# Kernel optimization log

Hardware: AMD Instinct MI355X
Metric: run time of the kernel (lower is better)

The kernel has to match this reference:

```python
import jax, jax.numpy as jnp
import numpy as np

B, S, D = 256, 512, 256
ATT = 128

def setup_inputs() -> dict:
    key = jax.random.key(0)
    k1, k2, k3, k4 = jax.random.split(key, 4)
    x = jax.random.normal(k1, (B, S, D), dtype=jnp.float32)
    W = jax.random.normal(k2, (D, ATT), dtype=jnp.float32)
    b = jax.random.normal(k3, (ATT,), dtype=jnp.float32)
    u = jax.random.normal(k4, (ATT, 1), dtype=jnp.float32)
    return {"x": x, "W": W, "b": b, "u": u}

def reference(x, W, b, u):
    # uit: [B, S, ATT]
    uit = jnp.tanh(jnp.einsum('bsd,da->bsa', x, W) + b)
    # scores: [B, S]  (faithful: exp without max-subtraction, as in original)
    ait = jnp.exp(jnp.einsum('bsa,a->bs', uit, u[:, 0]))
    ait = ait / (jnp.sum(ait, axis=1, keepdims=True) + 1e-08)
    # weighted sum over seq -> [B, D]
    return jnp.einsum('bsd,bs->bd', x, ait)
```

## Files before the change

### kernel.cpp

```cpp
#include <hip/hip_runtime.h>
#include <math.h>

typedef _Float16 f16x8 __attribute__((ext_vector_type(8)));
typedef float    f32x4 __attribute__((ext_vector_type(4)));

constexpr int B_ = 256, S_ = 512, D_ = 256, A_ = 128;
constexpr int BS = B_ * S_;

__device__ __forceinline__ float tanh_fast(float v) {
    return 1.0f - 2.0f / (1.0f + __expf(2.0f * v));
}

__global__ __launch_bounds__(512, 4) void k_scores(
    const float* __restrict__ x, const float* __restrict__ W,
    const float* __restrict__ bvec, const float* __restrict__ u,
    float* __restrict__ scores)
{
    __shared__ _Float16 xh[16 * 64 * 8];
    __shared__ _Float16 xl[16 * 64 * 8];
    __shared__ float    part[2][8][32];

    const int t    = threadIdx.x;
    const int lane = t & 63, wv = t >> 6;
    const int lr   = lane & 15, lg = lane >> 4;
    const int brow0 = blockIdx.x * 256;

    f16x8 Bh[8], Bl[8];
#pragma unroll
    for (int ks = 0; ks < 8; ++ks) {
        const float* wp = W + (size_t)(ks * 32 + lg * 8) * A_ + wv * 16 + lr;
#pragma unroll
        for (int i = 0; i < 8; ++i) {
            float v = wp[(size_t)i * A_];
            _Float16 h = (_Float16)v;
            Bh[ks][i] = h;
            Bl[ks][i] = (_Float16)(v - (float)h);
        }
    }
    const float bb = bvec[wv * 16 + lr];
    const float uu = u[wv * 16 + lr];

    float4 ld[2][2];

#define K1_ISSUE(TT)                                                              \
    {                                                                             \
        _Pragma("unroll")                                                         \
        for (int ff = 0; ff < 2; ++ff) {                                          \
            int f = wv * 2 + ff;                                                  \
            const float* p = x + (size_t)(brow0 + (TT) * 32 + ((f >> 3) << 4) + lr) * D_ \
                               + ((f & 7) << 5) + (lg << 3);                      \
            ld[ff][0] = *(const float4*)p;                                        \
            ld[ff][1] = *(const float4*)(p + 4);                                  \
        }                                                                         \
    }

#define K1_STAGE()                                                                \
    {                                                                             \
        _Pragma("unroll")                                                         \
        for (int ff = 0; ff < 2; ++ff) {                                          \
            int f = wv * 2 + ff;                                                  \
            float v[8] = {ld[ff][0].x, ld[ff][0].y, ld[ff][0].z, ld[ff][0].w,     \
                          ld[ff][1].x, ld[ff][1].y, ld[ff][1].z, ld[ff][1].w};    \
            f16x8 hi, lo;                                                         \
            _Pragma("unroll")                                                     \
            for (int i = 0; i < 8; ++i) {                                         \
                _Float16 h = (_Float16)v[i];                                      \
                hi[i] = h; lo[i] = (_Float16)(v[i] - (float)h);                   \
            }                                                                     \
            *(f16x8*)&xh[((size_t)f * 64 + lane) * 8] = hi;                       \
            *(f16x8*)&xl[((size_t)f * 64 + lane) * 8] = lo;                       \
        }                                                                         \
    }

    K1_ISSUE(0)
    K1_STAGE()

    for (int tt = 0; tt < 8; ++tt) {
        __syncthreads();
        if (tt > 0 && t < 32) {
            const float* pp = &part[(tt - 1) & 1][0][t];
            float ss = pp[0] + pp[32] + pp[64] + pp[96] + pp[128] + pp[160] + pp[192] + pp[224];
            scores[brow0 + (tt - 1) * 32 + t] = __expf(ss);
        }
        if (tt < 7) K1_ISSUE(tt + 1)

        f32x4 acc0 = {0.f, 0.f, 0.f, 0.f}, acc1 = {0.f, 0.f, 0.f, 0.f};
#pragma unroll
        for (int ks = 0; ks < 8; ++ks) {
            f16x8 ah0 = *(const f16x8*)&xh[((size_t)(ks) * 64 + lane) * 8];
            f16x8 al0 = *(const f16x8*)&xl[((size_t)(ks) * 64 + lane) * 8];
            f16x8 ah1 = *(const f16x8*)&xh[((size_t)(8 + ks) * 64 + lane) * 8];
            f16x8 al1 = *(const f16x8*)&xl[((size_t)(8 + ks) * 64 + lane) * 8];
            acc0 = __builtin_amdgcn_mfma_f32_16x16x32_f16(ah0, Bh[ks], acc0, 0, 0, 0);
            acc0 = __builtin_amdgcn_mfma_f32_16x16x32_f16(ah0, Bl[ks], acc0, 0, 0, 0);
            acc0 = __builtin_amdgcn_mfma_f32_16x16x32_f16(al0, Bh[ks], acc0, 0, 0, 0);
            acc1 = __builtin_amdgcn_mfma_f32_16x16x32_f16(ah1, Bh[ks], acc1, 0, 0, 0);
            acc1 = __builtin_amdgcn_mfma_f32_16x16x32_f16(ah1, Bl[ks], acc1, 0, 0, 0);
            acc1 = __builtin_amdgcn_mfma_f32_16x16x32_f16(al1, Bh[ks], acc1, 0, 0, 0);
        }
#pragma unroll
        for (int mt = 0; mt < 2; ++mt) {
            f32x4 a = mt ? acc1 : acc0;
#pragma unroll
            for (int r = 0; r < 4; ++r) {
                float s = tanh_fast(a[r] + bb) * uu;
                s += __shfl_xor(s, 8, 64);
                s += __shfl_xor(s, 4, 64);
                s += __shfl_xor(s, 2, 64);
                s += __shfl_xor(s, 1, 64);
                if (lr == 0) part[tt & 1][wv][mt * 16 + lg * 4 + r] = s;
            }
        }
        __syncthreads();
        if (tt < 7) K1_STAGE()
    }
    __syncthreads();
    if (t < 32) {
        const float* pp = &part[1][0][t];
        float ss = pp[0] + pp[32] + pp[64] + pp[96] + pp[128] + pp[160] + pp[192] + pp[224];
        scores[brow0 + 7 * 32 + t] = __expf(ss);
    }
#undef K1_ISSUE
#undef K1_STAGE
}

__global__ __launch_bounds__(512) void k_out(
    const float* __restrict__ x, const float* __restrict__ scores,
    float* __restrict__ out)
{
    __shared__ float sc[S_];
    __shared__ float red[8];
    __shared__ float pbuf[8][D_];

    const int t = threadIdx.x, b = blockIdx.x;
    const int lane = t & 63, w = t >> 6;

    float v = scores[(size_t)b * S_ + t];
    sc[t] = v;
    float rv = v;
#pragma unroll
    for (int m = 32; m >= 1; m >>= 1) rv += __shfl_xor(rv, m, 64);
    if (lane == 0) red[w] = rv;
    __syncthreads();

    const float* xp = x + ((size_t)b * S_ + (size_t)w * 64) * D_ + lane * 4;
    f32x4 a0 = {0.f, 0.f, 0.f, 0.f}, a1 = {0.f, 0.f, 0.f, 0.f};
#pragma unroll 8
    for (int j = 0; j < 64; j += 2) {
        float4 xa = *(const float4*)(xp + (size_t)j * D_);
        float4 xb = *(const float4*)(xp + (size_t)(j + 1) * D_);
        float s0 = sc[w * 64 + j], s1 = sc[w * 64 + j + 1];
        a0[0] = fmaf(xa.x, s0, a0[0]); a0[1] = fmaf(xa.y, s0, a0[1]);
        a0[2] = fmaf(xa.z, s0, a0[2]); a0[3] = fmaf(xa.w, s0, a0[3]);
        a1[0] = fmaf(xb.x, s1, a1[0]); a1[1] = fmaf(xb.y, s1, a1[1]);
        a1[2] = fmaf(xb.z, s1, a1[2]); a1[3] = fmaf(xb.w, s1, a1[3]);
    }
    a0[0] += a1[0]; a0[1] += a1[1]; a0[2] += a1[2]; a0[3] += a1[3];
    *(f32x4*)&pbuf[w][lane * 4] = a0;
    __syncthreads();

    if (t < D_) {
        float denom = 0.f;
#pragma unroll
        for (int i = 0; i < 8; ++i) denom += red[i];
        const float inv = 1.0f / (denom + 1e-8f);
        float r = 0.f;
#pragma unroll
        for (int i = 0; i < 8; ++i) r += pbuf[i][t];
        out[b * D_ + t] = r * inv;
    }
}

extern "C" void kernel_launch(void* const* d_in, const int* in_sizes, int n_in,
                              void* d_out, int out_size, void* d_ws, size_t ws_size,
                              hipStream_t stream)
{
    const float* x    = (const float*)d_in[0];
    const float* W    = (const float*)d_in[1];
    const float* bvec = (const float*)d_in[2];
    const float* u    = (const float*)d_in[3];
    float* out = (float*)d_out;
    float* scores = (float*)d_ws;

    k_scores<<<512, 512, 0, stream>>>(x, W, bvec, u, scores);
    k_out   <<<B_, 512, 0, stream>>>(x, scores, out);
}
```

Baseline: 224.5 us.

## Fuse score and weighted-sum kernels into one per-batch block

Merges the two kernels into one where each block handles a full batch row of 512 positions: it computes scores into shared memory, then normalises and does the weighted sum over x. This removes the global scores round trip and a kernel launch, and the second pass over x may hit in L2/MALL since the same block just read it. In exchange the grid shrinks from 512 to 256 blocks (one per batch) and the occupancy hint drops to 2, which lowers parallelism on a large GPU and may leave compute units idle.

```diff
diff --git a/kernel.cpp b/kernel.cpp
--- a/kernel.cpp
+++ b/kernel.cpp
@@ -5,25 +5,28 @@
 typedef float    f32x4 __attribute__((ext_vector_type(4)));
 
 constexpr int B_ = 256, S_ = 512, D_ = 256, A_ = 128;
-constexpr int BS = B_ * S_;
 
 __device__ __forceinline__ float tanh_fast(float v) {
     return 1.0f - 2.0f / (1.0f + __expf(2.0f * v));
 }
 
-__global__ __launch_bounds__(512, 4) void k_scores(
+__global__ __launch_bounds__(512, 2) void k_fused(
     const float* __restrict__ x, const float* __restrict__ W,
     const float* __restrict__ bvec, const float* __restrict__ u,
-    float* __restrict__ scores)
+    float* __restrict__ out)
 {
     __shared__ _Float16 xh[16 * 64 * 8];
     __shared__ _Float16 xl[16 * 64 * 8];
     __shared__ float    part[2][8][32];
+    __shared__ float    sc[S_];
+    __shared__ float    red[8];
+    __shared__ float    pbuf[8][D_];
 
     const int t    = threadIdx.x;
     const int lane = t & 63, wv = t >> 6;
     const int lr   = lane & 15, lg = lane >> 4;
-    const int brow0 = blockIdx.x * 256;
+    const int b    = blockIdx.x;
+    const float* __restrict__ xb = x + (size_t)b * S_ * D_;
 
     f16x8 Bh[8], Bl[8];
 #pragma unroll
@@ -47,8 +50,8 @@
         _Pragma("unroll")                                                         \
         for (int ff = 0; ff < 2; ++ff) {                                          \
             int f = wv * 2 + ff;                                                  \
-            const float* p = x + (size_t)(brow0 + (TT) * 32 + ((f >> 3) << 4) + lr) * D_ \
-                               + ((f & 7) << 5) + (lg << 3);                      \
+            const float* p = xb + (size_t)((TT) * 32 + ((f >> 3) << 4) + lr) * D_ \
+                                + ((f & 7) << 5) + (lg << 3);                     \
             ld[ff][0] = *(const float4*)p;                                        \
             ld[ff][1] = *(const float4*)(p + 4);                                  \
         }                                                                         \
@@ -75,14 +78,14 @@
     K1_ISSUE(0)
     K1_STAGE()
 
-    for (int tt = 0; tt < 8; ++tt) {
+    for (int tt = 0; tt < 16; ++tt) {
         __syncthreads();
         if (tt > 0 && t < 32) {
             const float* pp = &part[(tt - 1) & 1][0][t];
             float ss = pp[0] + pp[32] + pp[64] + pp[96] + pp[128] + pp[160] + pp[192] + pp[224];
-            scores[brow0 + (tt - 1) * 32 + t] = __expf(ss);
+            sc[(tt - 1) * 32 + t] = __expf(ss);
         }
-        if (tt < 7) K1_ISSUE(tt + 1)
+        if (tt < 15) K1_ISSUE(tt + 1)
 
         f32x4 acc0 = {0.f, 0.f, 0.f, 0.f}, acc1 = {0.f, 0.f, 0.f, 0.f};
 #pragma unroll
@@ -112,58 +115,46 @@
             }
         }
         __syncthreads();
-        if (tt < 7) K1_STAGE()
+        if (tt < 15) K1_STAGE()
     }
-    __syncthreads();
     if (t < 32) {
         const float* pp = &part[1][0][t];
         float ss = pp[0] + pp[32] + pp[64] + pp[96] + pp[128] + pp[160] + pp[192] + pp[224];
-        scores[brow0 + 7 * 32 + t] = __expf(ss);
+        sc[15 * 32 + t] = __expf(ss);
     }
+    __syncthreads();
 #undef K1_ISSUE
 #undef K1_STAGE
-}
 
-__global__ __launch_bounds__(512) void k_out(
-    const float* __restrict__ x, const float* __restrict__ scores,
-    float* __restrict__ out)
-{
-    __shared__ float sc[S_];
-    __shared__ float red[8];
-    __shared__ float pbuf[8][D_];
+    {
+        float v = sc[wv * 64 + lane];
+#pragma unroll
+        for (int m = 32; m >= 1; m >>= 1) v += __shfl_xor(v, m, 64);
+        if (lane == 0) red[wv] = v;
+    }
+    __syncthreads();
+    float denom = 0.f;
+#pragma unroll
+    for (int i = 0; i < 8; ++i) denom += red[i];
+    const float inv = 1.0f / (denom + 1e-8f);
 
-    const int t = threadIdx.x, b = blockIdx.x;
-    const int lane = t & 63, w = t >> 6;
-
-    float v = scores[(size_t)b * S_ + t];
-    sc[t] = v;
-    float rv = v;
-#pragma unroll
-    for (int m = 32; m >= 1; m >>= 1) rv += __shfl_xor(rv, m, 64);
-    if (lane == 0) red[w] = rv;
-    __syncthreads();
-
-    const float* xp = x + ((size_t)b * S_ + (size_t)w * 64) * D_ + lane * 4;
+    const float* xp = xb + (size_t)(wv * 64) * D_ + lane * 4;
     f32x4 a0 = {0.f, 0.f, 0.f, 0.f}, a1 = {0.f, 0.f, 0.f, 0.f};
 #pragma unroll 8
     for (int j = 0; j < 64; j += 2) {
-        float4 xa = *(const float4*)(xp + (size_t)j * D_);
-        float4 xb = *(const float4*)(xp + (size_t)(j + 1) * D_);
-        float s0 = sc[w * 64 + j], s1 = sc[w * 64 + j + 1];
-        a0[0] = fmaf(xa.x, s0, a0[0]); a0[1] = fmaf(xa.y, s0, a0[1]);
-        a0[2] = fmaf(xa.z, s0, a0[2]); a0[3] = fmaf(xa.w, s0, a0[3]);
-        a1[0] = fmaf(xb.x, s1, a1[0]); a1[1] = fmaf(xb.y, s1, a1[1]);
-        a1[2] = fmaf(xb.z, s1, a1[2]); a1[3] = fmaf(xb.w, s1, a1[3]);
+        float4 va = *(const float4*)(xp + (size_t)j * D_);
+        float4 vb = *(const float4*)(xp + (size_t)(j + 1) * D_);
+        float s0 = sc[wv * 64 + j], s1 = sc[wv * 64 + j + 1];
+        a0[0] = fmaf(va.x, s0, a0[0]); a0[1] = fmaf(va.y, s0, a0[1]);
+        a0[2] = fmaf(va.z, s0, a0[2]); a0[3] = fmaf(va.w, s0, a0[3]);
+        a1[0] = fmaf(vb.x, s1, a1[0]); a1[1] = fmaf(vb.y, s1, a1[1]);
+        a1[2] = fmaf(vb.z, s1, a1[2]); a1[3] = fmaf(vb.w, s1, a1[3]);
     }
     a0[0] += a1[0]; a0[1] += a1[1]; a0[2] += a1[2]; a0[3] += a1[3];
-    *(f32x4*)&pbuf[w][lane * 4] = a0;
+    *(f32x4*)&pbuf[wv][lane * 4] = a0;
     __syncthreads();
 
     if (t < D_) {
-        float denom = 0.f;
-#pragma unroll
-        for (int i = 0; i < 8; ++i) denom += red[i];
-        const float inv = 1.0f / (denom + 1e-8f);
         float r = 0.f;
 #pragma unroll
         for (int i = 0; i < 8; ++i) r += pbuf[i][t];
@@ -180,8 +171,6 @@
     const float* bvec = (const float*)d_in[2];
     const float* u    = (const float*)d_in[3];
     float* out = (float*)d_out;
-    float* scores = (float*)d_ws;
 
-    k_scores<<<512, 512, 0, stream>>>(x, W, bvec, u, scores);
-    k_out   <<<B_, 512, 0, stream>>>(x, scores, out);
+    k_fused<<<B_, 512, 0, stream>>>(x, W, bvec, u, out);
 }
```

New measurement: 217.4 us. -3.2%, faster.
